# Kernel optimization log

Hardware: AMD Instinct MI355X
Metric: run time of the kernel (lower is better)

## Reference

```python
import jax, jax.numpy as jnp
import numpy as np

SPARSITY = 0.5  # fraction of weights kept (top-|value| fraction set to 1)


def setup_inputs() -> dict:
    key = jax.random.key(0)
    # Production-scale FFN weight: [d_model=4096, d_ff=16384] = 64M params (256 MB fp32)
    param = jax.random.normal(key, (4096, 16384), dtype=jnp.float32)
    return {"param": param}


def _get_subnet(scores, k):
    """Faithful translation of GetSubnet.forward: sort flattened scores,
    zero the bottom (1-k) fraction, set the top k fraction to 1."""
    n = scores.size
    j = int((1.0 - k) * n)  # static: depends only on shape + python float k
    idx = jnp.argsort(scores.ravel())  # ascending, same as torch .sort()
    # original clones then overwrites every element with 0 or 1 ->
    # equivalent to zeros with ones scattered at the top-(n-j) ranks
    flat = jnp.zeros((n,), dtype=scores.dtype).at[idx[j:]].set(1.0)
    return flat.reshape(scores.shape)


def reference(param):
    scores = jnp.abs(param)
    return _get_subnet(scores, SPARSITY)
```

## Files before the change

kernel.cpp:

```cpp
#include <hip/hip_runtime.h>
#include <stdint.h>

#define NT 256
#define SCAN_BLOCKS 2048
#define SAMPLE_BLOCKS 32
#define SAMPLE_PER_BLOCK 32768
#define SBINS 16384
#define MARGIN 2500u
#define ABINS 4096
#define CH_BLOCKS 64
#define B8_CAP 8192
#define TIE_CAP 256
#define UMASK 0x7fffffffu

enum {
  M_LO = 0,
  M_HI,
  M_BASE8,
  M_SPANA,
  M_NLESSLO,
  M_B8,
  M_CUMA,
  M_NB8,
  M_V,
  M_ITHR,
  M_FAIL,
  M_NMETA
};

__global__ void k_zero(uint32_t* p, int n) {
  int i = blockIdx.x * NT + threadIdx.x;
  if (i < n) p[i] = 0;
}

__global__ void k_sample(const uint32_t* __restrict__ param, long long n,
                         uint32_t* __restrict__ hist16) {
  __shared__ uint32_t h[SBINS];
  for (int i = threadIdx.x; i < SBINS; i += NT) h[i] = 0;
  __syncthreads();
  long long chunk = n / SAMPLE_BLOCKS;
  const uint4* p4 = (const uint4*)(param + (long long)blockIdx.x * chunk);
#pragma unroll 4
  for (int k = 0; k < SAMPLE_PER_BLOCK / 4; k += NT) {
    uint4 w = p4[k + threadIdx.x];
    atomicAdd(&h[(w.x & UMASK) >> 17], 1u);
    atomicAdd(&h[(w.y & UMASK) >> 17], 1u);
    atomicAdd(&h[(w.z & UMASK) >> 17], 1u);
    atomicAdd(&h[(w.w & UMASK) >> 17], 1u);
  }
  __syncthreads();
  for (int i = threadIdx.x; i < SBINS; i += NT) {
    uint32_t v = h[i];
    if (v) atomicAdd(&hist16[i], v);
  }
}

__global__ void k_bounds(const uint32_t* __restrict__ hist16, uint32_t* meta,
                         uint32_t sRank) {
  __shared__ uint32_t part[NT];
  __shared__ uint32_t sLo, sHi;
  const int PER = SBINS / NT;
  int lo = threadIdx.x * PER;
  uint32_t s = 0;
  for (int b = 0; b < PER; ++b) s += hist16[lo + b];
  part[threadIdx.x] = s;
  __syncthreads();
  for (int off = 1; off < NT; off <<= 1) {
    uint32_t y = (threadIdx.x >= (unsigned)off) ? part[threadIdx.x - off] : 0u;
    __syncthreads();
    part[threadIdx.x] += y;
    __syncthreads();
  }
  uint32_t cum = part[threadIdx.x] - s;
  uint32_t loR = sRank - MARGIN, hiR = sRank + MARGIN;
  for (int b = 0; b < PER; ++b) {
    uint32_t hv = hist16[lo + b];
    if (cum <= loR && loR < cum + hv) sLo = (uint32_t)(lo + b) << 17;
    if (cum <= hiR && hiR < cum + hv) sHi = (((uint32_t)(lo + b) + 1u) << 17) - 1u;
    cum += hv;
  }
  __syncthreads();
  if (threadIdx.x == 0) {
    uint32_t l = sLo, hh = sHi;
    meta[M_LO] = l;
    meta[M_HI] = hh;
    meta[M_BASE8] = l >> 8;
    uint32_t span = (hh >> 8) - (l >> 8) + 1u;
    if (span > ABINS) { meta[M_FAIL] = 1u; span = ABINS; }
    meta[M_SPANA] = span;
  }
}

__global__ void k_scan(const uint32_t* __restrict__ param, long long n4,
                       uint32_t* meta,
                       uint2* __restrict__ candBuf, uint32_t perBlockCap,
                       uint32_t* __restrict__ blockCounts,
                       float* __restrict__ out) {
  __shared__ uint32_t lcount;
  __shared__ uint32_t red[NT];
  if (threadIdx.x == 0) lcount = 0;
  __syncthreads();
  const uint32_t lo = meta[M_LO], hi = meta[M_HI];
  uint2* myRegion = candBuf + (size_t)blockIdx.x * perBlockCap;
  uint32_t nless = 0;
  const uint4* p4 = (const uint4*)param;
  float4* o4 = (float4*)out;
  long long stride = (long long)gridDim.x * NT;
  for (long long i = (long long)blockIdx.x * NT + threadIdx.x; i < n4; i += stride) {
    uint4 w = p4[i];
    uint32_t baseIdx = (uint32_t)(i << 2);
    uint32_t us[4] = { w.x & UMASK, w.y & UMASK, w.z & UMASK, w.w & UMASK };
    float4 r;
    float* rp = (float*)&r;
#pragma unroll
    for (int c = 0; c < 4; ++c) {
      uint32_t u = us[c];
      rp[c] = (u > hi) ? 1.0f : 0.0f;
      nless += (u < lo) ? 1u : 0u;
      if (u >= lo && u <= hi) {
        uint32_t p = atomicAdd(&lcount, 1u);
        if (p < perBlockCap) myRegion[p] = make_uint2(baseIdx + (uint32_t)c, u);
      }
    }
    o4[i] = r;
  }
  red[threadIdx.x] = nless;
  __syncthreads();
  for (int off = NT / 2; off > 0; off >>= 1) {
    if (threadIdx.x < (unsigned)off) red[threadIdx.x] += red[threadIdx.x + off];
    __syncthreads();
  }
  if (threadIdx.x == 0) {
    atomicAdd(&meta[M_NLESSLO], red[0]);
    blockCounts[blockIdx.x] = (lcount < perBlockCap) ? lcount : perBlockCap;
    if (lcount > perBlockCap) atomicOr(&meta[M_FAIL], 2u);
  }
}

__global__ void k_candhist(const uint2* __restrict__ candBuf, uint32_t perBlockCap,
                           const uint32_t* __restrict__ blockCounts,
                           const uint32_t* __restrict__ meta,
                           uint32_t* __restrict__ candHist) {
  __shared__ uint32_t h[ABINS];
  for (int i = threadIdx.x; i < ABINS; i += NT) h[i] = 0;
  __syncthreads();
  uint32_t base8 = meta[M_BASE8];
  const int RPG = SCAN_BLOCKS / CH_BLOCKS;
  for (int r = 0; r < RPG; ++r) {
    int reg = blockIdx.x * RPG + r;
    uint32_t cnt = blockCounts[reg];
    const uint2* myR = candBuf + (size_t)reg * perBlockCap;
    for (uint32_t i = threadIdx.x; i < cnt; i += NT) {
      uint32_t idx = (myR[i].y >> 8) - base8;
      if (idx >= ABINS) idx = ABINS - 1;
      atomicAdd(&h[idx], 1u);
    }
  }
  __syncthreads();
  uint32_t* outp = candHist + (size_t)blockIdx.x * ABINS;
  for (int i = threadIdx.x; i < ABINS; i += NT) outp[i] = h[i];
}

__global__ void k_reduceA(const uint32_t* __restrict__ candHist,
                          uint32_t* __restrict__ histA) {
  int b = blockIdx.x * NT + threadIdx.x;
  uint32_t s = 0;
#pragma unroll 8
  for (int g = 0; g < CH_BLOCKS; ++g) s += candHist[(size_t)g * ABINS + b];
  histA[b] = s;
}

__global__ void k_selectA(const uint32_t* __restrict__ histA, uint32_t* meta,
                          uint32_t jrank) {
  __shared__ uint32_t part[NT];
  uint32_t jl = jrank - meta[M_NLESSLO];
  const int PER = ABINS / NT;
  int lo = threadIdx.x * PER;
  uint32_t s = 0;
  for (int b = 0; b < PER; ++b) s += histA[lo + b];
  part[threadIdx.x] = s;
  __syncthreads();
  for (int off = 1; off < NT; off <<= 1) {
    uint32_t y = (threadIdx.x >= (unsigned)off) ? part[threadIdx.x - off] : 0u;
    __syncthreads();
    part[threadIdx.x] += y;
    __syncthreads();
  }
  uint32_t cum = part[threadIdx.x] - s;
  for (int b = 0; b < PER; ++b) {
    uint32_t hv = histA[lo + b];
    if (cum <= jl && jl < cum + hv) {
      meta[M_B8] = meta[M_BASE8] + (uint32_t)(lo + b);
      meta[M_CUMA] = cum;
    }
    cum += hv;
  }
}

__global__ void k_collectB(const uint2* __restrict__ candBuf, uint32_t perBlockCap,
                           const uint32_t* __restrict__ blockCounts,
                           uint32_t* meta, uint2* __restrict__ b8buf) {
  uint32_t b8 = meta[M_B8];
  uint32_t cnt = blockCounts[blockIdx.x];
  const uint2* myRegion = candBuf + (size_t)blockIdx.x * perBlockCap;
  for (uint32_t i = threadIdx.x; i < cnt; i += NT) {
    uint2 e = myRegion[i];
    if ((e.y >> 8) == b8) {
      uint32_t p = atomicAdd(&meta[M_NB8], 1u);
      if (p < B8_CAP) b8buf[p] = e;
    }
  }
}

__global__ void k_selB(const uint2* __restrict__ b8buf, uint32_t* meta,
                       uint32_t jrank) {
  __shared__ uint32_t h[256];
  __shared__ uint32_t tieIdx[TIE_CAP];
  __shared__ uint32_t tcount, sv, sntz;
  uint32_t nb = meta[M_NB8]; if (nb > B8_CAP) nb = B8_CAP;
  if (threadIdx.x < 256) h[threadIdx.x] = 0;
  if (threadIdx.x == 0) { tcount = 0; sv = 0; sntz = 0; }
  __syncthreads();
  for (uint32_t i = threadIdx.x; i < nb; i += NT)
    atomicAdd(&h[b8buf[i].y & 255u], 1u);
  __syncthreads();
  if (threadIdx.x == 0) {
    uint32_t r = jrank - meta[M_NLESSLO] - meta[M_CUMA];
    uint32_t b8 = meta[M_B8];
    uint32_t cum = 0;
    for (int b = 0; b < 256; ++b) {
      uint32_t hv = h[b];
      if (cum <= r && r < cum + hv) {
        sv = (b8 << 8) | (uint32_t)b;
        sntz = r - cum;
        meta[M_V] = sv;
        break;
      }
      cum += hv;
    }
  }
  __syncthreads();
  uint32_t v = sv, ntz = sntz;
  for (uint32_t i = threadIdx.x; i < nb; i += NT) {
    uint2 e = b8buf[i];
    if (e.y == v) {
      uint32_t p = atomicAdd(&tcount, 1u);
      if (p < TIE_CAP) tieIdx[p] = e.x;
    }
  }
  __syncthreads();
  uint32_t T = tcount; if (T > TIE_CAP) T = TIE_CAP;
  if (ntz == 0) {
    if (threadIdx.x == 0) meta[M_ITHR] = 0u;
  } else {
    for (uint32_t t = threadIdx.x; t < T; t += NT) {
      uint32_t my = tieIdx[t], rk = 0;
      for (uint32_t s2 = 0; s2 < T; ++s2) rk += (tieIdx[s2] < my) ? 1u : 0u;
      if (rk == ntz) meta[M_ITHR] = my;
    }
  }
}

__global__ void k_fixup(const uint2* __restrict__ candBuf, uint32_t perBlockCap,
                        const uint32_t* __restrict__ blockCounts,
                        const uint32_t* __restrict__ meta,
                        float* __restrict__ out) {
  uint32_t v = meta[M_V], it = meta[M_ITHR];
  uint32_t cnt = blockCounts[blockIdx.x];
  const uint2* myRegion = candBuf + (size_t)blockIdx.x * perBlockCap;
  for (uint32_t i = threadIdx.x; i < cnt; i += NT) {
    uint2 e = myRegion[i];
    out[e.x] = (e.y > v || (e.y == v && e.x >= it)) ? 1.0f : 0.0f;
  }
}

extern "C" void kernel_launch(void* const* d_in, const int* in_sizes, int n_in,
                              void* d_out, int out_size, void* d_ws, size_t ws_size,
                              hipStream_t stream) {
  const uint32_t* param = (const uint32_t*)d_in[0];
  float* out = (float*)d_out;
  long long n = (long long)in_sizes[0];
  long long n4 = n >> 2;
  uint32_t jrank = (uint32_t)(n / 2);
  unsigned long long sTotal = (unsigned long long)SAMPLE_BLOCKS * SAMPLE_PER_BLOCK;
  uint32_t sRank = (uint32_t)(((unsigned long long)jrank * sTotal) / (unsigned long long)n);

  uint32_t* meta     = (uint32_t*)d_ws;
  uint32_t* hist16   = meta + 64;
  uint32_t* candHist = hist16 + SBINS;
  uint32_t* histA    = candHist + (size_t)CH_BLOCKS * ABINS;
  uint32_t* blockCounts = histA + ABINS;
  uint2* b8buf = (uint2*)(blockCounts + SCAN_BLOCKS);
  uint2* candBuf = b8buf + B8_CAP;
  size_t fixedBytes = ((size_t)64 + SBINS + (size_t)CH_BLOCKS * ABINS + ABINS +
                       SCAN_BLOCKS) * 4 + (size_t)B8_CAP * 8;

  uint32_t perBlockCap = 0;
  if (ws_size > fixedBytes + 8) {
    size_t slots = (ws_size - fixedBytes) / 8 / SCAN_BLOCKS;
    if (slots > 4096) slots = 4096;
    perBlockCap = (uint32_t)slots;
  }

  const int nzero = 64 + SBINS;
  k_zero<<<(nzero + NT - 1) / NT, NT, 0, stream>>>(meta, nzero);
  k_sample<<<SAMPLE_BLOCKS, NT, 0, stream>>>(param, n, hist16);
  k_bounds<<<1, NT, 0, stream>>>(hist16, meta, sRank);
  k_scan<<<SCAN_BLOCKS, NT, 0, stream>>>(param, n4, meta, candBuf, perBlockCap,
                                         blockCounts, out);
  k_candhist<<<CH_BLOCKS, NT, 0, stream>>>(candBuf, perBlockCap, blockCounts,
                                           meta, candHist);
  k_reduceA<<<ABINS / NT, NT, 0, stream>>>(candHist, histA);
  k_selectA<<<1, NT, 0, stream>>>(histA, meta, jrank);
  k_collectB<<<SCAN_BLOCKS, NT, 0, stream>>>(candBuf, perBlockCap, blockCounts,
                                             meta, b8buf);
  k_selB<<<1, NT, 0, stream>>>(b8buf, meta, jrank);
  k_fixup<<<SCAN_BLOCKS, NT, 0, stream>>>(candBuf, perBlockCap, blockCounts,
                                          meta, out);
}
```

Before: 235.6 us.

## Fuse selection stages into fewer kernels with coarser two-level radix bins

Cuts the post-scan selection pipeline from six kernels to three. A 256-bin coarse histogram over 11-bit buckets replaces the 4096-bin one. Every collect block redundantly reduces that histogram and picks the target bin, then gathers matching candidates through a shared-memory staging buffer. Every fixup block redundantly computes the exact threshold and tie index from a 2048-bin fine histogram. Per-block nless counts replace a global atomic, and sampling is spread over 64 blocks. The aim is to remove launch and serialization overhead from single-block kernels, at the cost of repeated per-block work and new capacity limits (LBUF_CAP, RBINS) that may overflow silently.

```diff
diff --git a/kernel.cpp b/kernel.cpp
--- a/kernel.cpp
+++ b/kernel.cpp
@@ -3,27 +3,26 @@
 
 #define NT 256
 #define SCAN_BLOCKS 2048
-#define SAMPLE_BLOCKS 32
-#define SAMPLE_PER_BLOCK 32768
+#define SAMPLE_BLOCKS 64
+#define SAMPLES_PER_BLOCK 16384
 #define SBINS 16384
 #define MARGIN 2500u
-#define ABINS 4096
-#define CH_BLOCKS 64
+#define RBINS 256
+#define REDUCE_BLOCKS 64
+#define COLLECT_BLOCKS 256
+#define LBUF_CAP 512
 #define B8_CAP 8192
 #define TIE_CAP 256
+#define FBINS 2048
 #define UMASK 0x7fffffffu
 
 enum {
   M_LO = 0,
   M_HI,
-  M_BASE8,
-  M_SPANA,
-  M_NLESSLO,
-  M_B8,
+  M_NB8,
+  M_BINB,
   M_CUMA,
-  M_NB8,
-  M_V,
-  M_ITHR,
+  M_NLESS,
   M_FAIL,
   M_NMETA
 };
@@ -41,7 +40,7 @@
   long long chunk = n / SAMPLE_BLOCKS;
   const uint4* p4 = (const uint4*)(param + (long long)blockIdx.x * chunk);
 #pragma unroll 4
-  for (int k = 0; k < SAMPLE_PER_BLOCK / 4; k += NT) {
+  for (int k = 0; k < SAMPLES_PER_BLOCK / 4; k += NT) {
     uint4 w = p4[k + threadIdx.x];
     atomicAdd(&h[(w.x & UMASK) >> 17], 1u);
     atomicAdd(&h[(w.y & UMASK) >> 17], 1u);
@@ -81,20 +80,17 @@
   }
   __syncthreads();
   if (threadIdx.x == 0) {
-    uint32_t l = sLo, hh = sHi;
-    meta[M_LO] = l;
-    meta[M_HI] = hh;
-    meta[M_BASE8] = l >> 8;
-    uint32_t span = (hh >> 8) - (l >> 8) + 1u;
-    if (span > ABINS) { meta[M_FAIL] = 1u; span = ABINS; }
-    meta[M_SPANA] = span;
+    meta[M_LO] = sLo;
+    meta[M_HI] = sHi;
+    if (((sHi >> 11) - (sLo >> 11) + 1u) > RBINS) meta[M_FAIL] = 1u;
   }
 }
 
 __global__ void k_scan(const uint32_t* __restrict__ param, long long n4,
-                       uint32_t* meta,
+                       const uint32_t* __restrict__ meta,
                        uint2* __restrict__ candBuf, uint32_t perBlockCap,
                        uint32_t* __restrict__ blockCounts,
+                       uint32_t* __restrict__ blockNless,
                        float* __restrict__ out) {
   __shared__ uint32_t lcount;
   __shared__ uint32_t red[NT];
@@ -131,54 +127,64 @@
     __syncthreads();
   }
   if (threadIdx.x == 0) {
-    atomicAdd(&meta[M_NLESSLO], red[0]);
+    blockNless[blockIdx.x] = red[0];
     blockCounts[blockIdx.x] = (lcount < perBlockCap) ? lcount : perBlockCap;
-    if (lcount > perBlockCap) atomicOr(&meta[M_FAIL], 2u);
-  }
-}
-
-__global__ void k_candhist(const uint2* __restrict__ candBuf, uint32_t perBlockCap,
-                           const uint32_t* __restrict__ blockCounts,
-                           const uint32_t* __restrict__ meta,
-                           uint32_t* __restrict__ candHist) {
-  __shared__ uint32_t h[ABINS];
-  for (int i = threadIdx.x; i < ABINS; i += NT) h[i] = 0;
-  __syncthreads();
-  uint32_t base8 = meta[M_BASE8];
-  const int RPG = SCAN_BLOCKS / CH_BLOCKS;
+  }
+}
+
+__global__ void k_reduce(const uint2* __restrict__ candBuf, uint32_t perBlockCap,
+                         const uint32_t* __restrict__ blockCounts,
+                         const uint32_t* __restrict__ meta,
+                         uint32_t* __restrict__ candHist2) {
+  __shared__ uint32_t h[RBINS];
+  for (int i = threadIdx.x; i < RBINS; i += NT) h[i] = 0;
+  __syncthreads();
+  uint32_t base11 = meta[M_LO] >> 11;
+  const int RPG = SCAN_BLOCKS / REDUCE_BLOCKS;
   for (int r = 0; r < RPG; ++r) {
     int reg = blockIdx.x * RPG + r;
     uint32_t cnt = blockCounts[reg];
-    const uint2* myR = candBuf + (size_t)reg * perBlockCap;
+    const uint2* my = candBuf + (size_t)reg * perBlockCap;
     for (uint32_t i = threadIdx.x; i < cnt; i += NT) {
-      uint32_t idx = (myR[i].y >> 8) - base8;
-      if (idx >= ABINS) idx = ABINS - 1;
-      atomicAdd(&h[idx], 1u);
-    }
-  }
-  __syncthreads();
-  uint32_t* outp = candHist + (size_t)blockIdx.x * ABINS;
-  for (int i = threadIdx.x; i < ABINS; i += NT) outp[i] = h[i];
-}
-
-__global__ void k_reduceA(const uint32_t* __restrict__ candHist,
-                          uint32_t* __restrict__ histA) {
-  int b = blockIdx.x * NT + threadIdx.x;
-  uint32_t s = 0;
-#pragma unroll 8
-  for (int g = 0; g < CH_BLOCKS; ++g) s += candHist[(size_t)g * ABINS + b];
-  histA[b] = s;
-}
-
-__global__ void k_selectA(const uint32_t* __restrict__ histA, uint32_t* meta,
+      uint32_t rel = (my[i].y >> 11) - base11;
+      if (rel >= RBINS) rel = RBINS - 1;
+      atomicAdd(&h[rel], 1u);
+    }
+  }
+  __syncthreads();
+  for (int b = threadIdx.x; b < RBINS; b += NT)
+    candHist2[(size_t)b * REDUCE_BLOCKS + blockIdx.x] = h[b];
+}
+
+__global__ void k_collect(const uint2* __restrict__ candBuf, uint32_t perBlockCap,
+                          const uint32_t* __restrict__ blockCounts,
+                          const uint32_t* __restrict__ blockNless,
+                          const uint32_t* __restrict__ candHist2,
+                          uint32_t* meta, uint2* __restrict__ b8buf,
                           uint32_t jrank) {
+  __shared__ uint32_t histA[RBINS];
   __shared__ uint32_t part[NT];
-  uint32_t jl = jrank - meta[M_NLESSLO];
-  const int PER = ABINS / NT;
-  int lo = threadIdx.x * PER;
-  uint32_t s = 0;
-  for (int b = 0; b < PER; ++b) s += histA[lo + b];
-  part[threadIdx.x] = s;
+  __shared__ uint32_t sBin, sCum;
+  __shared__ uint2 lbuf[LBUF_CAP];
+  __shared__ uint32_t lcnt, base;
+  {
+    uint32_t s = 0;
+    const uint32_t* row = candHist2 + (size_t)threadIdx.x * REDUCE_BLOCKS;
+    for (int g = 0; g < REDUCE_BLOCKS; ++g) s += row[g];
+    histA[threadIdx.x] = s;
+  }
+  uint32_t ns = 0;
+  for (int i = threadIdx.x; i < SCAN_BLOCKS; i += NT) ns += blockNless[i];
+  part[threadIdx.x] = ns;
+  __syncthreads();
+  for (int off = NT / 2; off > 0; off >>= 1) {
+    if (threadIdx.x < (unsigned)off) part[threadIdx.x] += part[threadIdx.x + off];
+    __syncthreads();
+  }
+  uint32_t nless = part[0];
+  __syncthreads();
+  uint32_t h = histA[threadIdx.x];
+  part[threadIdx.x] = h;
   __syncthreads();
   for (int off = 1; off < NT; off <<= 1) {
     uint32_t y = (threadIdx.x >= (unsigned)off) ? part[threadIdx.x - off] : 0u;
@@ -186,90 +192,98 @@
     part[threadIdx.x] += y;
     __syncthreads();
   }
-  uint32_t cum = part[threadIdx.x] - s;
-  for (int b = 0; b < PER; ++b) {
-    uint32_t hv = histA[lo + b];
-    if (cum <= jl && jl < cum + hv) {
-      meta[M_B8] = meta[M_BASE8] + (uint32_t)(lo + b);
-      meta[M_CUMA] = cum;
-    }
-    cum += hv;
-  }
-}
-
-__global__ void k_collectB(const uint2* __restrict__ candBuf, uint32_t perBlockCap,
-                           const uint32_t* __restrict__ blockCounts,
-                           uint32_t* meta, uint2* __restrict__ b8buf) {
-  uint32_t b8 = meta[M_B8];
-  uint32_t cnt = blockCounts[blockIdx.x];
-  const uint2* myRegion = candBuf + (size_t)blockIdx.x * perBlockCap;
-  for (uint32_t i = threadIdx.x; i < cnt; i += NT) {
-    uint2 e = myRegion[i];
-    if ((e.y >> 8) == b8) {
-      uint32_t p = atomicAdd(&meta[M_NB8], 1u);
-      if (p < B8_CAP) b8buf[p] = e;
-    }
-  }
-}
-
-__global__ void k_selB(const uint2* __restrict__ b8buf, uint32_t* meta,
-                       uint32_t jrank) {
-  __shared__ uint32_t h[256];
-  __shared__ uint32_t tieIdx[TIE_CAP];
-  __shared__ uint32_t tcount, sv, sntz;
-  uint32_t nb = meta[M_NB8]; if (nb > B8_CAP) nb = B8_CAP;
-  if (threadIdx.x < 256) h[threadIdx.x] = 0;
-  if (threadIdx.x == 0) { tcount = 0; sv = 0; sntz = 0; }
-  __syncthreads();
-  for (uint32_t i = threadIdx.x; i < nb; i += NT)
-    atomicAdd(&h[b8buf[i].y & 255u], 1u);
-  __syncthreads();
+  uint32_t jl = jrank - nless;
+  uint32_t cum = part[threadIdx.x] - h;
+  if (threadIdx.x == 0) lcnt = 0;
+  if (cum <= jl && jl < cum + h) { sBin = threadIdx.x; sCum = cum; }
+  __syncthreads();
+  uint32_t binB = sBin;
   if (threadIdx.x == 0) {
-    uint32_t r = jrank - meta[M_NLESSLO] - meta[M_CUMA];
-    uint32_t b8 = meta[M_B8];
-    uint32_t cum = 0;
-    for (int b = 0; b < 256; ++b) {
-      uint32_t hv = h[b];
-      if (cum <= r && r < cum + hv) {
-        sv = (b8 << 8) | (uint32_t)b;
-        sntz = r - cum;
-        meta[M_V] = sv;
-        break;
+    meta[M_BINB] = binB; meta[M_CUMA] = sCum; meta[M_NLESS] = nless;
+  }
+  uint32_t base11 = meta[M_LO] >> 11;
+  const int RPG = SCAN_BLOCKS / COLLECT_BLOCKS;
+  for (int r = 0; r < RPG; ++r) {
+    int reg = blockIdx.x * RPG + r;
+    uint32_t cnt = blockCounts[reg];
+    const uint2* my = candBuf + (size_t)reg * perBlockCap;
+    for (uint32_t i = threadIdx.x; i < cnt; i += NT) {
+      uint2 e = my[i];
+      if (((e.y >> 11) - base11) == binB) {
+        uint32_t p = atomicAdd(&lcnt, 1u);
+        if (p < LBUF_CAP) lbuf[p] = e;
       }
-      cum += hv;
-    }
-  }
-  __syncthreads();
-  uint32_t v = sv, ntz = sntz;
-  for (uint32_t i = threadIdx.x; i < nb; i += NT) {
-    uint2 e = b8buf[i];
-    if (e.y == v) {
-      uint32_t p = atomicAdd(&tcount, 1u);
-      if (p < TIE_CAP) tieIdx[p] = e.x;
-    }
-  }
-  __syncthreads();
-  uint32_t T = tcount; if (T > TIE_CAP) T = TIE_CAP;
-  if (ntz == 0) {
-    if (threadIdx.x == 0) meta[M_ITHR] = 0u;
-  } else {
-    for (uint32_t t = threadIdx.x; t < T; t += NT) {
-      uint32_t my = tieIdx[t], rk = 0;
-      for (uint32_t s2 = 0; s2 < T; ++s2) rk += (tieIdx[s2] < my) ? 1u : 0u;
-      if (rk == ntz) meta[M_ITHR] = my;
-    }
+    }
+  }
+  __syncthreads();
+  uint32_t c = (lcnt < LBUF_CAP) ? lcnt : LBUF_CAP;
+  if (threadIdx.x == 0) base = atomicAdd(&meta[M_NB8], c);
+  __syncthreads();
+  for (uint32_t i = threadIdx.x; i < c; i += NT) {
+    uint32_t p = base + i;
+    if (p < B8_CAP) b8buf[p] = lbuf[i];
   }
 }
 
 __global__ void k_fixup(const uint2* __restrict__ candBuf, uint32_t perBlockCap,
                         const uint32_t* __restrict__ blockCounts,
                         const uint32_t* __restrict__ meta,
-                        float* __restrict__ out) {
-  uint32_t v = meta[M_V], it = meta[M_ITHR];
+                        const uint2* __restrict__ b8buf,
+                        float* __restrict__ out, uint32_t jrank) {
+  __shared__ uint32_t h[FBINS];
+  __shared__ uint32_t part[NT];
+  __shared__ uint32_t tie[TIE_CAP];
+  __shared__ uint32_t tcnt, sV, sNtz, sIthr;
+  for (int i = threadIdx.x; i < FBINS; i += NT) h[i] = 0;
+  if (threadIdx.x == 0) { tcnt = 0; sIthr = 0; sNtz = 0; }
+  __syncthreads();
+  uint32_t nb = meta[M_NB8]; if (nb > B8_CAP) nb = B8_CAP;
+  uint32_t vbase = ((meta[M_LO] >> 11) + meta[M_BINB]) << 11;
+  for (uint32_t i = threadIdx.x; i < nb; i += NT)
+    atomicAdd(&h[b8buf[i].y & (FBINS - 1)], 1u);
+  __syncthreads();
+  const int PER = FBINS / NT;
+  uint32_t loB = threadIdx.x * PER, s = 0;
+  for (int b = 0; b < PER; ++b) s += h[loB + b];
+  part[threadIdx.x] = s;
+  __syncthreads();
+  for (int off = 1; off < NT; off <<= 1) {
+    uint32_t y = (threadIdx.x >= (unsigned)off) ? part[threadIdx.x - off] : 0u;
+    __syncthreads();
+    part[threadIdx.x] += y;
+    __syncthreads();
+  }
+  uint32_t jl2 = jrank - meta[M_NLESS] - meta[M_CUMA];
+  uint32_t cum = part[threadIdx.x] - s;
+  for (int b = 0; b < PER; ++b) {
+    uint32_t hv = h[loB + b];
+    if (cum <= jl2 && jl2 < cum + hv) { sV = vbase + loB + (uint32_t)b; sNtz = jl2 - cum; }
+    cum += hv;
+  }
+  __syncthreads();
+  uint32_t v = sV, ntz = sNtz;
+  if (ntz) {
+    for (uint32_t i = threadIdx.x; i < nb; i += NT) {
+      uint2 e = b8buf[i];
+      if (e.y == v) {
+        uint32_t p = atomicAdd(&tcnt, 1u);
+        if (p < TIE_CAP) tie[p] = e.x;
+      }
+    }
+    __syncthreads();
+    uint32_t T = (tcnt < TIE_CAP) ? tcnt : TIE_CAP;
+    for (uint32_t t = threadIdx.x; t < T; t += NT) {
+      uint32_t my = tie[t], rk = 0;
+      for (uint32_t q = 0; q < T; ++q) rk += (tie[q] < my) ? 1u : 0u;
+      if (rk == ntz) sIthr = my;
+    }
+    __syncthreads();
+  }
+  uint32_t it = sIthr;
   uint32_t cnt = blockCounts[blockIdx.x];
-  const uint2* myRegion = candBuf + (size_t)blockIdx.x * perBlockCap;
+  const uint2* my = candBuf + (size_t)blockIdx.x * perBlockCap;
   for (uint32_t i = threadIdx.x; i < cnt; i += NT) {
-    uint2 e = myRegion[i];
+    uint2 e = my[i];
     out[e.x] = (e.y > v || (e.y == v && e.x >= it)) ? 1.0f : 0.0f;
   }
 }
@@ -282,18 +296,18 @@
   long long n = (long long)in_sizes[0];
   long long n4 = n >> 2;
   uint32_t jrank = (uint32_t)(n / 2);
-  unsigned long long sTotal = (unsigned long long)SAMPLE_BLOCKS * SAMPLE_PER_BLOCK;
+  unsigned long long sTotal = (unsigned long long)SAMPLE_BLOCKS * SAMPLES_PER_BLOCK;
   uint32_t sRank = (uint32_t)(((unsigned long long)jrank * sTotal) / (unsigned long long)n);
 
-  uint32_t* meta     = (uint32_t*)d_ws;
-  uint32_t* hist16   = meta + 64;
-  uint32_t* candHist = hist16 + SBINS;
-  uint32_t* histA    = candHist + (size_t)CH_BLOCKS * ABINS;
-  uint32_t* blockCounts = histA + ABINS;
-  uint2* b8buf = (uint2*)(blockCounts + SCAN_BLOCKS);
+  uint32_t* meta      = (uint32_t*)d_ws;
+  uint32_t* hist16    = meta + 64;
+  uint32_t* candHist2 = hist16 + SBINS;
+  uint32_t* blockCounts = candHist2 + RBINS * REDUCE_BLOCKS;
+  uint32_t* blockNless  = blockCounts + SCAN_BLOCKS;
+  uint2* b8buf = (uint2*)(blockNless + SCAN_BLOCKS);
   uint2* candBuf = b8buf + B8_CAP;
-  size_t fixedBytes = ((size_t)64 + SBINS + (size_t)CH_BLOCKS * ABINS + ABINS +
-                       SCAN_BLOCKS) * 4 + (size_t)B8_CAP * 8;
+  size_t fixedBytes = ((size_t)64 + SBINS + RBINS * REDUCE_BLOCKS +
+                       2 * SCAN_BLOCKS) * 4 + (size_t)B8_CAP * 8;
 
   uint32_t perBlockCap = 0;
   if (ws_size > fixedBytes + 8) {
@@ -302,19 +316,17 @@
     perBlockCap = (uint32_t)slots;
   }
 
-  const int nzero = 64 + SBINS;
+  const int nzero = 64 + SBINS + RBINS * REDUCE_BLOCKS;
   k_zero<<<(nzero + NT - 1) / NT, NT, 0, stream>>>(meta, nzero);
   k_sample<<<SAMPLE_BLOCKS, NT, 0, stream>>>(param, n, hist16);
   k_bounds<<<1, NT, 0, stream>>>(hist16, meta, sRank);
   k_scan<<<SCAN_BLOCKS, NT, 0, stream>>>(param, n4, meta, candBuf, perBlockCap,
-                                         blockCounts, out);
-  k_candhist<<<CH_BLOCKS, NT, 0, stream>>>(candBuf, perBlockCap, blockCounts,
-                                           meta, candHist);
-  k_reduceA<<<ABINS / NT, NT, 0, stream>>>(candHist, histA);
-  k_selectA<<<1, NT, 0, stream>>>(histA, meta, jrank);
-  k_collectB<<<SCAN_BLOCKS, NT, 0, stream>>>(candBuf, perBlockCap, blockCounts,
-                                             meta, b8buf);
-  k_selB<<<1, NT, 0, stream>>>(b8buf, meta, jrank);
+                                         blockCounts, blockNless, out);
+  k_reduce<<<REDUCE_BLOCKS, NT, 0, stream>>>(candBuf, perBlockCap, blockCounts,
+                                             meta, candHist2);
+  k_collect<<<COLLECT_BLOCKS, NT, 0, stream>>>(candBuf, perBlockCap, blockCounts,
+                                               blockNless, candHist2, meta,
+                                               b8buf, jrank);
   k_fixup<<<SCAN_BLOCKS, NT, 0, stream>>>(candBuf, perBlockCap, blockCounts,
-                                          meta, out);
-}
+                                          meta, b8buf, out, jrank);
+}
```

After: 235.2 us. No clear change (-0.2%).
